# Optimization experiments

Hardware: AMD Instinct MI355X
Metric: run time of the kernel (lower is better)

Reference implementation:

```python
import jax, jax.numpy as jnp
import numpy as np

DIM, HEADS, HEAD_DIM = 1024, 16, 64
B, S = 2, 1024
LAMBDA = 4.0
EPS = 1e-6


def setup_inputs() -> dict:
    key = jax.random.key(0)
    ks = jax.random.split(key, 7)
    sc = 1.0 / np.sqrt(DIM)
    return {
        "x": jax.random.normal(ks[0], (B, S, DIM), jnp.float32),
        "qkv_w": jax.random.normal(ks[1], (3 * DIM, DIM), jnp.float32) * sc,
        "qkv_b": jax.random.normal(ks[2], (3 * DIM,), jnp.float32) * 0.01,
        "proj_w": jax.random.normal(ks[3], (DIM, DIM), jnp.float32) * sc,
        "proj_b": jax.random.normal(ks[4], (DIM,), jnp.float32) * 0.01,
        "dwc_w": jax.random.normal(ks[5], (DIM, 1, 3), jnp.float32) * 0.3,
        "dwc_b": jax.random.normal(ks[6], (DIM,), jnp.float32) * 0.01,
    }


def _l1_dist(q, k):
    # q,k: [B,H,S,Dh] -> pairwise L1 distance [B,H,S,S].
    # Accumulate over head_dim with a (rematerialized) scan so we never
    # materialize the [B,H,S,S,Dh] broadcast tensor.
    qT = jnp.moveaxis(q, -1, 0)  # [Dh,B,H,S]
    kT = jnp.moveaxis(k, -1, 0)

    def step(acc, qk):
        qd, kd = qk  # [B,H,S]
        return acc + jnp.abs(qd[..., :, None] - kd[..., None, :]), None

    init = jnp.zeros(q.shape[:-1] + (k.shape[-2],), q.dtype)
    dist, _ = jax.lax.scan(jax.checkpoint(step), init, (qT, kT))
    return dist


def reference(x, qkv_w, qkv_b, proj_w, proj_b, dwc_w, dwc_b):
    Bq, Sq, C = x.shape
    # qkv projection -> q,k,v each [B,H,S,Dh]
    qkv = (x @ qkv_w.T + qkv_b).reshape(Bq, Sq, 3, HEADS, HEAD_DIM)
    qkv = jnp.transpose(qkv, (2, 0, 3, 1, 4))
    q, k, v = qkv[0], qkv[1], qkv[2]

    # exact Laplacian (L1-distance) kernel attention, row-normalized
    dist = _l1_dist(q, k)                       # [B,H,S,S]
    kern = jnp.exp(-LAMBDA * dist / HEAD_DIM)   # mean-L1 scaling
    attn = kern / (jnp.sum(kern, axis=-1, keepdims=True) + EPS)
    global_attn = jnp.einsum("bhij,bhjd->bhid", attn, v)

    # depthwise conv1d local branch on v (channel order = head-major)
    v1d = jnp.transpose(v, (0, 1, 3, 2)).reshape(Bq, C, Sq)  # [B,C,S]
    local = jax.lax.conv_general_dilated(
        v1d, dwc_w, window_strides=(1,), padding=((1, 1),),
        feature_group_count=C, dimension_numbers=("NCH", "OIH", "NCH"))
    local = local + dwc_b[None, :, None]
    local = jnp.transpose(local.reshape(Bq, HEADS, HEAD_DIM, Sq), (0, 1, 3, 2))

    y = global_attn + local                      # [B,H,S,Dh]
    y = jnp.transpose(y, (0, 2, 1, 3)).reshape(Bq, Sq, C)
    return y @ proj_w.T + proj_b
```

## Files before the change

kernel.cpp:

```cpp
#include <hip/hip_runtime.h>

#define DIMC 1024
#define HEADS 16
#define HD 64
#define BATCH 2
#define SEQ 1024
#define NQKV 3072

typedef _Float16 f16;
typedef _Float16 half8 __attribute__((ext_vector_type(8)));
typedef _Float16 half4v __attribute__((ext_vector_type(4)));
typedef float floatx4 __attribute__((ext_vector_type(4)));

__device__ __forceinline__ void gld16(const void* g, void* l) {
  __builtin_amdgcn_global_load_lds((const __attribute__((address_space(1))) void*)g,
                                   (__attribute__((address_space(3))) void*)l, 16, 0, 0);
}

__device__ __forceinline__ unsigned sadU8(unsigned a, unsigned b, unsigned c) {
#if __has_builtin(__builtin_amdgcn_sad_u8)
  return __builtin_amdgcn_sad_u8(a, b, c);
#else
  unsigned d;
  asm("v_sad_u8 %0, %1, %2, %3" : "=v"(d) : "v"(a), "v"(b), "v"(c));
  return d;
#endif
}

__global__ __launch_bounds__(256) void cvt_kernel(
    const float* __restrict__ x, const float* __restrict__ wq, const float* __restrict__ wp,
    f16* __restrict__ x16, f16* __restrict__ wq16, f16* __restrict__ wp16)
{
  long long bid = blockIdx.x;
  const float* src; f16* dst; long long base;
  if (bid < 2048)            { src = x;  dst = x16;  base = bid; }
  else if (bid < 2048+3072)  { src = wq; dst = wq16; base = bid - 2048; }
  else                       { src = wp; dst = wp16; base = bid - (2048+3072); }
  long long i = base*256 + threadIdx.x;
  float4 v = ((const float4*)src)[i];
  half4v h; h[0]=(f16)v.x; h[1]=(f16)v.y; h[2]=(f16)v.z; h[3]=(f16)v.w;
  *(half4v*)(dst + i*4) = h;
}

template<int MODE>
__global__ __launch_bounds__(256, 2) void gemm_kernel(
    const f16* __restrict__ A, const f16* __restrict__ Bw, const float* __restrict__ bias,
    unsigned char* __restrict__ q8, unsigned char* __restrict__ k8, f16* __restrict__ vT,
    float* __restrict__ outp, int K)
{
  __shared__ f16 As[128*64];
  __shared__ f16 Bs[128*64];
  const int tid = threadIdx.x;
  const int wave = tid >> 6, lane = tid & 63;
  const int lq = lane >> 4, li = lane & 15;
  const int m0 = blockIdx.y * 128, n0 = blockIdx.x * 128;
  const int wm = (wave & 1) * 64, wn = (wave >> 1) * 64;
  floatx4 acc[4][4] = {};

  const int kIters = K / 64;
  for (int kt = 0; kt < kIters; ++kt) {
    __syncthreads();
#pragma unroll
    for (int r = 0; r < 4; ++r) {
      int slot = r*256 + tid;
      int row = slot >> 3, c = slot & 7, sc = c ^ (row & 7);
      gld16(A  + (size_t)(m0+row)*K + kt*64 + sc*8, As + slot*8);
      gld16(Bw + (size_t)(n0+row)*K + kt*64 + sc*8, Bs + slot*8);
    }
    __syncthreads();
#pragma unroll
    for (int ks = 0; ks < 2; ++ks) {
      half8 af[4], bf[4];
#pragma unroll
      for (int t = 0; t < 4; ++t) {
        int am = wm + t*16 + li;
        int kc = ks*4 + lq;
        af[t] = *(const half8*)&As[am*64 + (kc ^ (am & 7))*8];
        int bn = wn + t*16 + li;
        bf[t] = *(const half8*)&Bs[bn*64 + (kc ^ (bn & 7))*8];
      }
#pragma unroll
      for (int mt = 0; mt < 4; ++mt)
#pragma unroll
        for (int nt = 0; nt < 4; ++nt)
          acc[mt][nt] = __builtin_amdgcn_mfma_f32_16x16x32_f16(af[mt], bf[nt], acc[mt][nt], 0, 0, 0);
    }
  }

#pragma unroll
  for (int mt = 0; mt < 4; ++mt) {
#pragma unroll
    for (int nt = 0; nt < 4; ++nt) {
      int f = n0 + wn + nt*16 + li;
      float bb = bias[f];
      if (MODE == 0) {
        int which = f >> 10, cc = f & 1023, h = cc >> 6, d = cc & 63;
        int t0 = m0 + wm + mt*16 + lq*4;
        int b = t0 >> 10, s0 = t0 & 1023;
        if (which == 2) {
          half4v hv;
#pragma unroll
          for (int r = 0; r < 4; ++r) hv[r] = (f16)(acc[mt][nt][r] + bb);
          *(half4v*)&vT[((size_t)((b*HEADS + h)*HD + d))*SEQ + s0] = hv;
        } else {
          unsigned char* dst = (which == 0) ? q8 : k8;
#pragma unroll
          for (int r = 0; r < 4; ++r) {
            float v = acc[mt][nt][r] + bb;
            int u = (int)floorf(v * 16.0f + 128.5f);
            u = u < 0 ? 0 : (u > 255 ? 255 : u);
            dst[((size_t)((b*HEADS + h)*SEQ + s0 + r))*HD + d] = (unsigned char)u;
          }
        }
      } else {
#pragma unroll
        for (int r = 0; r < 4; ++r) {
          int t = m0 + wm + mt*16 + lq*4 + r;
          outp[(size_t)t*DIMC + f] = acc[mt][nt][r] + bb;
        }
      }
    }
  }
}

__global__ __launch_bounds__(256, 2) void attn_kernel(
    const unsigned char* __restrict__ q8g, const unsigned char* __restrict__ k8g,
    const f16* __restrict__ vTg, const float* __restrict__ dwcw, const float* __restrict__ dwcb,
    f16* __restrict__ y16)
{
  __shared__ unsigned char q8s[64*64];
  __shared__ unsigned char k8s[128*64];
  __shared__ f16 vTs[64*128];
  __shared__ f16 sfrag[16*64*8];
  __shared__ float rspart[64*16];
  __shared__ float rowsum[64];
  __shared__ f16 vconv[64*66];

  const int tid = threadIdx.x;
  const int bh = blockIdx.y;
  const int i0 = blockIdx.x * 64;
  const int lane = tid & 63, wave = tid >> 6;
  const int lq = lane >> 4, li = lane & 15;
  const int iL = tid & 15, jt = tid >> 4;
  const int ksj = jt >> 2, qj = jt & 3;

  {
    int row = tid >> 2, c = tid & 3;
    gld16(q8g + ((size_t)(bh*SEQ) + i0 + row)*HD + c*16, q8s + tid*16);
  }
  {
    int d = tid >> 2, part = tid & 3;
    const f16* vrow = vTg + ((size_t)(bh*HD) + d)*SEQ;
#pragma unroll
    for (int e = 0; e < 17; ++e) {
      int ss = part*17 + e;
      if (ss < 66) {
        int s = i0 - 1 + ss;
        vconv[d*66 + ss] = (s >= 0 && s < SEQ) ? vrow[s] : (f16)0.0f;
      }
    }
  }
  __syncthreads();

  unsigned qr[4][16];
#pragma unroll
  for (int n = 0; n < 4; ++n)
#pragma unroll
    for (int c4 = 0; c4 < 4; ++c4) {
      uint4 t = *(const uint4*)&q8s[(iL + n*16)*64 + c4*16];
      qr[n][c4*4+0] = t.x; qr[n][c4*4+1] = t.y; qr[n][c4*4+2] = t.z; qr[n][c4*4+3] = t.w;
    }

  float rs[4] = {0.f, 0.f, 0.f, 0.f};
  floatx4 pacc[2][2] = {};
  const int mtb = (wave & 1) * 2, ntb = (wave >> 1) * 2;

  for (int jb = 0; jb < 8; ++jb) {
    const int j0 = jb * 128;
    __syncthreads();
#pragma unroll
    for (int r = 0; r < 2; ++r) {
      int slot = r*256 + tid;
      int row = slot >> 2, c = slot & 3;
      gld16(k8g + ((size_t)(bh*SEQ) + j0 + row)*HD + c*16, k8s + slot*16);
    }
#pragma unroll
    for (int r = 0; r < 4; ++r) {
      int slot = r*256 + tid;
      int d = slot >> 4, c = slot & 15, sc = c ^ (d & 7);
      gld16(vTg + ((size_t)(bh*HD) + d)*SEQ + j0 + sc*8, vTs + slot*8);
    }
    __syncthreads();

    unsigned sacc[4][8] = {};
#pragma unroll
    for (int c4 = 0; c4 < 4; ++c4) {
      uint4 kk[8];
#pragma unroll
      for (int jj = 0; jj < 8; ++jj)
        kk[jj] = *(const uint4*)&k8s[(jt*8 + jj)*64 + c4*16];
#pragma unroll
      for (int n = 0; n < 4; ++n)
#pragma unroll
        for (int jj = 0; jj < 8; ++jj) {
          sacc[n][jj] = sadU8(qr[n][c4*4+0], kk[jj].x, sacc[n][jj]);
          sacc[n][jj] = sadU8(qr[n][c4*4+1], kk[jj].y, sacc[n][jj]);
          sacc[n][jj] = sadU8(qr[n][c4*4+2], kk[jj].z, sacc[n][jj]);
          sacc[n][jj] = sadU8(qr[n][c4*4+3], kk[jj].w, sacc[n][jj]);
        }
    }
#pragma unroll
    for (int n = 0; n < 4; ++n) {
      half8 sv;
#pragma unroll
      for (int jj = 0; jj < 8; ++jj) {
        float sf = exp2f(-0.0056355275f * (float)sacc[n][jj]);
        rs[n] += sf;
        sv[jj] = (f16)sf;
      }
      *(half8*)&sfrag[((n*4 + ksj)*64 + qj*16 + iL)*8] = sv;
    }
    __syncthreads();

#pragma unroll
    for (int ks = 0; ks < 4; ++ks) {
      half8 a0 = *(const half8*)&sfrag[(((mtb+0)*4 + ks)*64 + lane)*8];
      half8 a1 = *(const half8*)&sfrag[(((mtb+1)*4 + ks)*64 + lane)*8];
#pragma unroll
      for (int nt = 0; nt < 2; ++nt) {
        int d = (ntb + nt)*16 + li;
        int kc = ks*4 + lq;
        half8 bfr = *(const half8*)&vTs[d*128 + (kc ^ (d & 7))*8];
        pacc[0][nt] = __builtin_amdgcn_mfma_f32_16x16x32_f16(a0, bfr, pacc[0][nt], 0, 0, 0);
        pacc[1][nt] = __builtin_amdgcn_mfma_f32_16x16x32_f16(a1, bfr, pacc[1][nt], 0, 0, 0);
      }
    }
  }

#pragma unroll
  for (int n = 0; n < 4; ++n) rspart[(iL + n*16)*16 + jt] = rs[n];
  __syncthreads();
  if (tid < 64) {
    float s = 0.f;
#pragma unroll
    for (int t = 0; t < 16; ++t) s += rspart[tid*16 + t];
    rowsum[tid] = s + 1e-6f;
  }
  __syncthreads();

  const int b = bh >> 4, h = bh & 15;
#pragma unroll
  for (int nt = 0; nt < 2; ++nt) {
    int d = (ntb + nt)*16 + li;
    int c = h*64 + d;
    float w0 = dwcw[c*3+0], w1 = dwcw[c*3+1], w2 = dwcw[c*3+2], cb = dwcb[c];
#pragma unroll
    for (int mt = 0; mt < 2; ++mt)
#pragma unroll
      for (int r = 0; r < 4; ++r) {
        int ii = (mtb + mt)*16 + lq*4 + r;
        float val = pacc[mt][nt][r] / rowsum[ii];
        val += w0*(float)vconv[d*66 + ii] + w1*(float)vconv[d*66 + ii + 1]
             + w2*(float)vconv[d*66 + ii + 2] + cb;
        int s = i0 + ii;
        y16[((size_t)(b*SEQ + s))*DIMC + c] = (f16)val;
      }
  }
}

extern "C" void kernel_launch(void* const* d_in, const int* in_sizes, int n_in,
                              void* d_out, int out_size, void* d_ws, size_t ws_size,
                              hipStream_t stream) {
  const float* x      = (const float*)d_in[0];
  const float* qkv_w  = (const float*)d_in[1];
  const float* qkv_b  = (const float*)d_in[2];
  const float* proj_w = (const float*)d_in[3];
  const float* proj_b = (const float*)d_in[4];
  const float* dwc_w  = (const float*)d_in[5];
  const float* dwc_b  = (const float*)d_in[6];
  float* out = (float*)d_out;

  char* ws = (char*)d_ws;
  f16* x16  = (f16*)(ws);
  f16* wq16 = (f16*)(ws + (4ll<<20));
  f16* wp16 = (f16*)(ws + (10ll<<20));
  unsigned char* q8 = (unsigned char*)(ws + (12ll<<20));
  unsigned char* k8 = (unsigned char*)(ws + (14ll<<20));
  f16* vT   = (f16*)(ws + (16ll<<20));
  f16* y16  = (f16*)(ws + (20ll<<20));

  cvt_kernel<<<6144, 256, 0, stream>>>(x, qkv_w, proj_w, x16, wq16, wp16);
  gemm_kernel<0><<<dim3(24, 16), 256, 0, stream>>>(x16, wq16, qkv_b, q8, k8, vT, nullptr, DIMC);
  attn_kernel<<<dim3(16, 32), 256, 0, stream>>>(q8, k8, vT, dwc_w, dwc_b, y16);
  gemm_kernel<1><<<dim3(8, 16), 256, 0, stream>>>(y16, wp16, proj_b, nullptr, nullptr, nullptr, out, DIMC);
}
```

Before: 163.3 us.

## Split attention keys across waves with double-buffered staging; shrink GEMM tiles

The attention kernel now gives each wave its own quarter of the key sequence. K/V tiles are double-buffered with per-wave async loads and explicit waitcnt instead of block-wide barriers. Score fragments go straight from registers into MFMA operands rather than through shared memory, and per-wave partial outputs and row sums are combined with LDS atomics at the end. The GEMMs are templated on tile size and use smaller 64x128 and 64x64 tiles with higher occupancy bounds, to fill more CUs. The cost is an LDS atomic reduction over 64x64 floats, reloading q from LDS on every step, and more register pressure from the 4x4 accumulators.

After: 194.1 us. 18.9% more time.

```diff
diff --git a/kernel.cpp b/kernel.cpp
--- a/kernel.cpp
+++ b/kernel.cpp
@@ -42,55 +42,65 @@
   *(half4v*)(dst + i*4) = h;
 }
 
-template<int MODE>
-__global__ __launch_bounds__(256, 2) void gemm_kernel(
+template<int TM, int TN, int MODE>
+__global__ __launch_bounds__(256, 4) void gemm_kernel(
     const f16* __restrict__ A, const f16* __restrict__ Bw, const float* __restrict__ bias,
     unsigned char* __restrict__ q8, unsigned char* __restrict__ k8, f16* __restrict__ vT,
     float* __restrict__ outp, int K)
 {
-  __shared__ f16 As[128*64];
-  __shared__ f16 Bs[128*64];
+  constexpr int MT = TM / 32;
+  constexpr int NT = TN / 32;
+  __shared__ f16 As[TM*64];
+  __shared__ f16 Bs[TN*64];
   const int tid = threadIdx.x;
   const int wave = tid >> 6, lane = tid & 63;
   const int lq = lane >> 4, li = lane & 15;
-  const int m0 = blockIdx.y * 128, n0 = blockIdx.x * 128;
-  const int wm = (wave & 1) * 64, wn = (wave >> 1) * 64;
-  floatx4 acc[4][4] = {};
+  const int m0 = blockIdx.y * TM, n0 = blockIdx.x * TN;
+  const int wm = (wave & 1) * (TM/2), wn = (wave >> 1) * (TN/2);
+  floatx4 acc[MT][NT] = {};
 
   const int kIters = K / 64;
   for (int kt = 0; kt < kIters; ++kt) {
     __syncthreads();
 #pragma unroll
-    for (int r = 0; r < 4; ++r) {
+    for (int r = 0; r < TM/32; ++r) {
       int slot = r*256 + tid;
       int row = slot >> 3, c = slot & 7, sc = c ^ (row & 7);
-      gld16(A  + (size_t)(m0+row)*K + kt*64 + sc*8, As + slot*8);
+      gld16(A + (size_t)(m0+row)*K + kt*64 + sc*8, As + slot*8);
+    }
+#pragma unroll
+    for (int r = 0; r < TN/32; ++r) {
+      int slot = r*256 + tid;
+      int row = slot >> 3, c = slot & 7, sc = c ^ (row & 7);
       gld16(Bw + (size_t)(n0+row)*K + kt*64 + sc*8, Bs + slot*8);
     }
     __syncthreads();
 #pragma unroll
     for (int ks = 0; ks < 2; ++ks) {
-      half8 af[4], bf[4];
-#pragma unroll
-      for (int t = 0; t < 4; ++t) {
+      half8 af[MT], bf[NT];
+      int kc = ks*4 + lq;
+#pragma unroll
+      for (int t = 0; t < MT; ++t) {
         int am = wm + t*16 + li;
-        int kc = ks*4 + lq;
         af[t] = *(const half8*)&As[am*64 + (kc ^ (am & 7))*8];
+      }
+#pragma unroll
+      for (int t = 0; t < NT; ++t) {
         int bn = wn + t*16 + li;
         bf[t] = *(const half8*)&Bs[bn*64 + (kc ^ (bn & 7))*8];
       }
 #pragma unroll
-      for (int mt = 0; mt < 4; ++mt)
-#pragma unroll
-        for (int nt = 0; nt < 4; ++nt)
+      for (int mt = 0; mt < MT; ++mt)
+#pragma unroll
+        for (int nt = 0; nt < NT; ++nt)
           acc[mt][nt] = __builtin_amdgcn_mfma_f32_16x16x32_f16(af[mt], bf[nt], acc[mt][nt], 0, 0, 0);
     }
   }
 
 #pragma unroll
-  for (int mt = 0; mt < 4; ++mt) {
-#pragma unroll
-    for (int nt = 0; nt < 4; ++nt) {
+  for (int mt = 0; mt < MT; ++mt) {
+#pragma unroll
+    for (int nt = 0; nt < NT; ++nt) {
       int f = n0 + wn + nt*16 + li;
       float bb = bias[f];
       if (MODE == 0) {
@@ -129,11 +139,10 @@
     f16* __restrict__ y16)
 {
   __shared__ unsigned char q8s[64*64];
-  __shared__ unsigned char k8s[128*64];
-  __shared__ f16 vTs[64*128];
-  __shared__ f16 sfrag[16*64*8];
-  __shared__ float rspart[64*16];
-  __shared__ float rowsum[64];
+  __shared__ unsigned char k8s[2][4][32*64];
+  __shared__ f16 vTs[2][4][64*32];
+  __shared__ float Obuf[64*64];
+  __shared__ float rowsumS[64];
   __shared__ f16 vconv[64*66];
 
   const int tid = threadIdx.x;
@@ -141,13 +150,13 @@
   const int i0 = blockIdx.x * 64;
   const int lane = tid & 63, wave = tid >> 6;
   const int lq = lane >> 4, li = lane & 15;
-  const int iL = tid & 15, jt = tid >> 4;
-  const int ksj = jt >> 2, qj = jt & 3;
-
-  {
-    int row = tid >> 2, c = tid & 3;
-    gld16(q8g + ((size_t)(bh*SEQ) + i0 + row)*HD + c*16, q8s + tid*16);
-  }
+
+#pragma unroll
+  for (int i = 0; i < 16; ++i) Obuf[tid + i*256] = 0.0f;
+  if (tid < 64) rowsumS[tid] = 1e-6f;
+
+  gld16(q8g + ((size_t)bh*SEQ + i0)*HD + tid*16, q8s + tid*16);
+
   {
     int d = tid >> 2, part = tid & 3;
     const f16* vrow = vTg + ((size_t)(bh*HD) + d)*SEQ;
@@ -160,112 +169,122 @@
       }
     }
   }
+
+  auto stage = [&](int buf, int jb) {
+    int j0w = wave*256 + jb*32;
+    const unsigned char* kg = k8g + ((size_t)bh*SEQ + j0w)*HD;
+    unsigned char* kd = &k8s[buf][wave][0];
+    gld16(kg + lane*16,        kd + lane*16);
+    gld16(kg + 1024 + lane*16, kd + 1024 + lane*16);
+    f16* vd = &vTs[buf][wave][0];
+#pragma unroll
+    for (int i4 = 0; i4 < 4; ++i4) {
+      int d = i4*16 + (lane >> 2), c = lane & 3;
+      int g = c ^ ((d >> 1) & 3);
+      gld16(vTg + ((size_t)(bh*HD) + d)*SEQ + j0w + g*8, vd + i4*512 + lane*8);
+    }
+  };
+
+  stage(0, 0);
   __syncthreads();
 
-  unsigned qr[4][16];
-#pragma unroll
-  for (int n = 0; n < 4; ++n)
-#pragma unroll
-    for (int c4 = 0; c4 < 4; ++c4) {
-      uint4 t = *(const uint4*)&q8s[(iL + n*16)*64 + c4*16];
-      qr[n][c4*4+0] = t.x; qr[n][c4*4+1] = t.y; qr[n][c4*4+2] = t.z; qr[n][c4*4+3] = t.w;
-    }
-
   float rs[4] = {0.f, 0.f, 0.f, 0.f};
-  floatx4 pacc[2][2] = {};
-  const int mtb = (wave & 1) * 2, ntb = (wave >> 1) * 2;
+  floatx4 pacc[4][4] = {};
 
   for (int jb = 0; jb < 8; ++jb) {
-    const int j0 = jb * 128;
-    __syncthreads();
-#pragma unroll
-    for (int r = 0; r < 2; ++r) {
-      int slot = r*256 + tid;
-      int row = slot >> 2, c = slot & 3;
-      gld16(k8g + ((size_t)(bh*SEQ) + j0 + row)*HD + c*16, k8s + slot*16);
-    }
-#pragma unroll
-    for (int r = 0; r < 4; ++r) {
-      int slot = r*256 + tid;
-      int d = slot >> 4, c = slot & 15, sc = c ^ (d & 7);
-      gld16(vTg + ((size_t)(bh*HD) + d)*SEQ + j0 + sc*8, vTs + slot*8);
-    }
-    __syncthreads();
+    int cur = jb & 1;
+    if (jb < 7) {
+      stage(cur ^ 1, jb + 1);
+      __builtin_amdgcn_sched_barrier(0);
+      __builtin_amdgcn_s_waitcnt(0x0F76);
+    } else {
+      __builtin_amdgcn_sched_barrier(0);
+      __builtin_amdgcn_s_waitcnt(0x0F70);
+    }
+    __builtin_amdgcn_sched_barrier(0);
+
+    const unsigned char* kb = &k8s[cur][wave][0];
+    const f16* vb = &vTs[cur][wave][0];
 
     unsigned sacc[4][8] = {};
 #pragma unroll
-    for (int c4 = 0; c4 < 4; ++c4) {
+    for (int p = 0; p < 4; ++p) {
+      int cc = (p + lq) & 3;
       uint4 kk[8];
 #pragma unroll
       for (int jj = 0; jj < 8; ++jj)
-        kk[jj] = *(const uint4*)&k8s[(jt*8 + jj)*64 + c4*16];
+        kk[jj] = *(const uint4*)&kb[(lq*8 + jj)*64 + cc*16];
+      uint4 qc[4];
 #pragma unroll
       for (int n = 0; n < 4; ++n)
+        qc[n] = *(const uint4*)&q8s[(li + n*16)*64 + cc*16];
+#pragma unroll
+      for (int n = 0; n < 4; ++n)
 #pragma unroll
         for (int jj = 0; jj < 8; ++jj) {
-          sacc[n][jj] = sadU8(qr[n][c4*4+0], kk[jj].x, sacc[n][jj]);
-          sacc[n][jj] = sadU8(qr[n][c4*4+1], kk[jj].y, sacc[n][jj]);
-          sacc[n][jj] = sadU8(qr[n][c4*4+2], kk[jj].z, sacc[n][jj]);
-          sacc[n][jj] = sadU8(qr[n][c4*4+3], kk[jj].w, sacc[n][jj]);
+          sacc[n][jj] = sadU8(qc[n].x, kk[jj].x, sacc[n][jj]);
+          sacc[n][jj] = sadU8(qc[n].y, kk[jj].y, sacc[n][jj]);
+          sacc[n][jj] = sadU8(qc[n].z, kk[jj].z, sacc[n][jj]);
+          sacc[n][jj] = sadU8(qc[n].w, kk[jj].w, sacc[n][jj]);
         }
     }
-#pragma unroll
-    for (int n = 0; n < 4; ++n) {
-      half8 sv;
+
+    half8 af[4];
+#pragma unroll
+    for (int n = 0; n < 4; ++n)
 #pragma unroll
       for (int jj = 0; jj < 8; ++jj) {
         float sf = exp2f(-0.0056355275f * (float)sacc[n][jj]);
         rs[n] += sf;
-        sv[jj] = (f16)sf;
-      }
-      *(half8*)&sfrag[((n*4 + ksj)*64 + qj*16 + iL)*8] = sv;
-    }
-    __syncthreads();
-
-#pragma unroll
-    for (int ks = 0; ks < 4; ++ks) {
-      half8 a0 = *(const half8*)&sfrag[(((mtb+0)*4 + ks)*64 + lane)*8];
-      half8 a1 = *(const half8*)&sfrag[(((mtb+1)*4 + ks)*64 + lane)*8];
-#pragma unroll
-      for (int nt = 0; nt < 2; ++nt) {
-        int d = (ntb + nt)*16 + li;
-        int kc = ks*4 + lq;
-        half8 bfr = *(const half8*)&vTs[d*128 + (kc ^ (d & 7))*8];
-        pacc[0][nt] = __builtin_amdgcn_mfma_f32_16x16x32_f16(a0, bfr, pacc[0][nt], 0, 0, 0);
-        pacc[1][nt] = __builtin_amdgcn_mfma_f32_16x16x32_f16(a1, bfr, pacc[1][nt], 0, 0, 0);
-      }
-    }
-  }
-
-#pragma unroll
-  for (int n = 0; n < 4; ++n) rspart[(iL + n*16)*16 + jt] = rs[n];
+        af[n][jj] = (f16)sf;
+      }
+
+#pragma unroll
+    for (int nt = 0; nt < 4; ++nt) {
+      int d = nt*16 + li;
+      half8 bfr = *(const half8*)&vb[d*32 + ((lq ^ ((d >> 1) & 3)) * 8)];
+#pragma unroll
+      for (int mt = 0; mt < 4; ++mt)
+        pacc[mt][nt] = __builtin_amdgcn_mfma_f32_16x16x32_f16(af[mt], bfr, pacc[mt][nt], 0, 0, 0);
+    }
+  }
+
+#pragma unroll
+  for (int n = 0; n < 4; ++n) {
+    rs[n] += __shfl_xor(rs[n], 16, 64);
+    rs[n] += __shfl_xor(rs[n], 32, 64);
+  }
+  if (lane < 16) {
+#pragma unroll
+    for (int n = 0; n < 4; ++n) atomicAdd(&rowsumS[lane + n*16], rs[n]);
+  }
+#pragma unroll
+  for (int mt = 0; mt < 4; ++mt)
+#pragma unroll
+    for (int nt = 0; nt < 4; ++nt)
+#pragma unroll
+      for (int r = 0; r < 4; ++r)
+        atomicAdd(&Obuf[(mt*16 + lq*4 + r)*64 + nt*16 + li], pacc[mt][nt][r]);
   __syncthreads();
-  if (tid < 64) {
-    float s = 0.f;
-#pragma unroll
-    for (int t = 0; t < 16; ++t) s += rspart[tid*16 + t];
-    rowsum[tid] = s + 1e-6f;
-  }
-  __syncthreads();
 
   const int b = bh >> 4, h = bh & 15;
-#pragma unroll
-  for (int nt = 0; nt < 2; ++nt) {
-    int d = (ntb + nt)*16 + li;
+  const int r = tid >> 2, dq = tid & 3;
+  float inv = 1.0f / rowsumS[r];
+  half8 hv0, hv1;
+#pragma unroll
+  for (int e = 0; e < 16; ++e) {
+    int d = dq*16 + e;
     int c = h*64 + d;
-    float w0 = dwcw[c*3+0], w1 = dwcw[c*3+1], w2 = dwcw[c*3+2], cb = dwcb[c];
-#pragma unroll
-    for (int mt = 0; mt < 2; ++mt)
-#pragma unroll
-      for (int r = 0; r < 4; ++r) {
-        int ii = (mtb + mt)*16 + lq*4 + r;
-        float val = pacc[mt][nt][r] / rowsum[ii];
-        val += w0*(float)vconv[d*66 + ii] + w1*(float)vconv[d*66 + ii + 1]
-             + w2*(float)vconv[d*66 + ii + 2] + cb;
-        int s = i0 + ii;
-        y16[((size_t)(b*SEQ + s))*DIMC + c] = (f16)val;
-      }
-  }
+    float val = Obuf[r*64 + d] * inv
+              + dwcw[c*3+0] * (float)vconv[d*66 + r]
+              + dwcw[c*3+1] * (float)vconv[d*66 + r + 1]
+              + dwcw[c*3+2] * (float)vconv[d*66 + r + 2]
+              + dwcb[c];
+    if (e < 8) hv0[e] = (f16)val; else hv1[e-8] = (f16)val;
+  }
+  f16* yp = y16 + ((size_t)(b*SEQ + i0 + r))*DIMC + h*64 + dq*16;
+  *(half8*)yp = hv0;
+  *(half8*)(yp + 8) = hv1;
 }
 
 extern "C" void kernel_launch(void* const* d_in, const int* in_sizes, int n_in,
@@ -290,7 +309,7 @@
   f16* y16  = (f16*)(ws + (20ll<<20));
 
   cvt_kernel<<<6144, 256, 0, stream>>>(x, qkv_w, proj_w, x16, wq16, wp16);
-  gemm_kernel<0><<<dim3(24, 16), 256, 0, stream>>>(x16, wq16, qkv_b, q8, k8, vT, nullptr, DIMC);
+  gemm_kernel<64,128,0><<<dim3(24, 32), 256, 0, stream>>>(x16, wq16, qkv_b, q8, k8, vT, nullptr, DIMC);
   attn_kernel<<<dim3(16, 32), 256, 0, stream>>>(q8, k8, vT, dwc_w, dwc_b, y16);
-  gemm_kernel<1><<<dim3(8, 16), 256, 0, stream>>>(y16, wp16, proj_b, nullptr, nullptr, nullptr, out, DIMC);
-}
+  gemm_kernel<64,64,1><<<dim3(16, 32), 256, 0, stream>>>(y16, wp16, proj_b, nullptr, nullptr, nullptr, out, DIMC);
+}
```

## Shrink GEMM and attention tiles for more blocks; read V fragments directly from global

Applied to the files above, without the earlier changes.

Templates the GEMM on tile sizes and launches smaller tiles (64x128 for QKV, 64x64 for the projection) with a higher occupancy hint. This raises block count on a many-CU GPU. The attention kernel halves the query rows per block to 32, doubling the grid. It drops the LDS staging of V, so MFMA B-fragments are loaded straight from global memory. The aim is better CU utilisation and less LDS use, at the cost of more redundant K/V reads and uncoalesced global loads inside the MFMA loop.

Result: no change. 162.0 us (-0.8%).

```diff
diff --git a/kernel.cpp b/kernel.cpp
--- a/kernel.cpp
+++ b/kernel.cpp
@@ -42,55 +42,65 @@
   *(half4v*)(dst + i*4) = h;
 }
 
-template<int MODE>
-__global__ __launch_bounds__(256, 2) void gemm_kernel(
+template<int TM, int TN, int MODE>
+__global__ __launch_bounds__(256, 4) void gemm_kernel(
     const f16* __restrict__ A, const f16* __restrict__ Bw, const float* __restrict__ bias,
     unsigned char* __restrict__ q8, unsigned char* __restrict__ k8, f16* __restrict__ vT,
     float* __restrict__ outp, int K)
 {
-  __shared__ f16 As[128*64];
-  __shared__ f16 Bs[128*64];
+  constexpr int MT = TM / 32;
+  constexpr int NT = TN / 32;
+  __shared__ f16 As[TM*64];
+  __shared__ f16 Bs[TN*64];
   const int tid = threadIdx.x;
   const int wave = tid >> 6, lane = tid & 63;
   const int lq = lane >> 4, li = lane & 15;
-  const int m0 = blockIdx.y * 128, n0 = blockIdx.x * 128;
-  const int wm = (wave & 1) * 64, wn = (wave >> 1) * 64;
-  floatx4 acc[4][4] = {};
+  const int m0 = blockIdx.y * TM, n0 = blockIdx.x * TN;
+  const int wm = (wave & 1) * (TM/2), wn = (wave >> 1) * (TN/2);
+  floatx4 acc[MT][NT] = {};
 
   const int kIters = K / 64;
   for (int kt = 0; kt < kIters; ++kt) {
     __syncthreads();
 #pragma unroll
-    for (int r = 0; r < 4; ++r) {
+    for (int r = 0; r < TM/32; ++r) {
       int slot = r*256 + tid;
       int row = slot >> 3, c = slot & 7, sc = c ^ (row & 7);
-      gld16(A  + (size_t)(m0+row)*K + kt*64 + sc*8, As + slot*8);
+      gld16(A + (size_t)(m0+row)*K + kt*64 + sc*8, As + slot*8);
+    }
+#pragma unroll
+    for (int r = 0; r < TN/32; ++r) {
+      int slot = r*256 + tid;
+      int row = slot >> 3, c = slot & 7, sc = c ^ (row & 7);
       gld16(Bw + (size_t)(n0+row)*K + kt*64 + sc*8, Bs + slot*8);
     }
     __syncthreads();
 #pragma unroll
     for (int ks = 0; ks < 2; ++ks) {
-      half8 af[4], bf[4];
-#pragma unroll
-      for (int t = 0; t < 4; ++t) {
+      half8 af[MT], bf[NT];
+      int kc = ks*4 + lq;
+#pragma unroll
+      for (int t = 0; t < MT; ++t) {
         int am = wm + t*16 + li;
-        int kc = ks*4 + lq;
         af[t] = *(const half8*)&As[am*64 + (kc ^ (am & 7))*8];
+      }
+#pragma unroll
+      for (int t = 0; t < NT; ++t) {
         int bn = wn + t*16 + li;
         bf[t] = *(const half8*)&Bs[bn*64 + (kc ^ (bn & 7))*8];
       }
 #pragma unroll
-      for (int mt = 0; mt < 4; ++mt)
-#pragma unroll
-        for (int nt = 0; nt < 4; ++nt)
+      for (int mt = 0; mt < MT; ++mt)
+#pragma unroll
+        for (int nt = 0; nt < NT; ++nt)
           acc[mt][nt] = __builtin_amdgcn_mfma_f32_16x16x32_f16(af[mt], bf[nt], acc[mt][nt], 0, 0, 0);
     }
   }
 
 #pragma unroll
-  for (int mt = 0; mt < 4; ++mt) {
-#pragma unroll
-    for (int nt = 0; nt < 4; ++nt) {
+  for (int mt = 0; mt < MT; ++mt) {
+#pragma unroll
+    for (int nt = 0; nt < NT; ++nt) {
       int f = n0 + wn + nt*16 + li;
       float bb = bias[f];
       if (MODE == 0) {
@@ -123,57 +133,55 @@
   }
 }
 
-__global__ __launch_bounds__(256, 2) void attn_kernel(
+__global__ __launch_bounds__(256, 4) void attn_kernel(
     const unsigned char* __restrict__ q8g, const unsigned char* __restrict__ k8g,
     const f16* __restrict__ vTg, const float* __restrict__ dwcw, const float* __restrict__ dwcb,
     f16* __restrict__ y16)
 {
-  __shared__ unsigned char q8s[64*64];
+  __shared__ unsigned char q8s[32*64];
   __shared__ unsigned char k8s[128*64];
-  __shared__ f16 vTs[64*128];
-  __shared__ f16 sfrag[16*64*8];
-  __shared__ float rspart[64*16];
-  __shared__ float rowsum[64];
-  __shared__ f16 vconv[64*66];
+  __shared__ f16 sfrag[8*64*8];
+  __shared__ float rspart[32*16];
+  __shared__ float rowsumS[32];
+  __shared__ f16 vconv[64*34];
 
   const int tid = threadIdx.x;
   const int bh = blockIdx.y;
-  const int i0 = blockIdx.x * 64;
+  const int i0 = blockIdx.x * 32;
   const int lane = tid & 63, wave = tid >> 6;
   const int lq = lane >> 4, li = lane & 15;
   const int iL = tid & 15, jt = tid >> 4;
   const int ksj = jt >> 2, qj = jt & 3;
-
-  {
-    int row = tid >> 2, c = tid & 3;
-    gld16(q8g + ((size_t)(bh*SEQ) + i0 + row)*HD + c*16, q8s + tid*16);
-  }
+  const int mtb = wave & 1, ntb = wave >> 1;
+
+  if (wave < 2)
+    gld16(q8g + ((size_t)bh*SEQ + i0)*HD + tid*16, q8s + tid*16);
+
   {
     int d = tid >> 2, part = tid & 3;
     const f16* vrow = vTg + ((size_t)(bh*HD) + d)*SEQ;
 #pragma unroll
-    for (int e = 0; e < 17; ++e) {
-      int ss = part*17 + e;
-      if (ss < 66) {
+    for (int e = 0; e < 9; ++e) {
+      int ss = part*9 + e;
+      if (ss < 34) {
         int s = i0 - 1 + ss;
-        vconv[d*66 + ss] = (s >= 0 && s < SEQ) ? vrow[s] : (f16)0.0f;
+        vconv[d*34 + ss] = (s >= 0 && s < SEQ) ? vrow[s] : (f16)0.0f;
       }
     }
   }
   __syncthreads();
 
-  unsigned qr[4][16];
-#pragma unroll
-  for (int n = 0; n < 4; ++n)
+  unsigned qr[2][16];
+#pragma unroll
+  for (int n = 0; n < 2; ++n)
 #pragma unroll
     for (int c4 = 0; c4 < 4; ++c4) {
       uint4 t = *(const uint4*)&q8s[(iL + n*16)*64 + c4*16];
       qr[n][c4*4+0] = t.x; qr[n][c4*4+1] = t.y; qr[n][c4*4+2] = t.z; qr[n][c4*4+3] = t.w;
     }
 
-  float rs[4] = {0.f, 0.f, 0.f, 0.f};
-  floatx4 pacc[2][2] = {};
-  const int mtb = (wave & 1) * 2, ntb = (wave >> 1) * 2;
+  float rs[2] = {0.f, 0.f};
+  floatx4 pacc[2] = {};
 
   for (int jb = 0; jb < 8; ++jb) {
     const int j0 = jb * 128;
@@ -181,18 +189,11 @@
 #pragma unroll
     for (int r = 0; r < 2; ++r) {
       int slot = r*256 + tid;
-      int row = slot >> 2, c = slot & 3;
-      gld16(k8g + ((size_t)(bh*SEQ) + j0 + row)*HD + c*16, k8s + slot*16);
-    }
-#pragma unroll
-    for (int r = 0; r < 4; ++r) {
-      int slot = r*256 + tid;
-      int d = slot >> 4, c = slot & 15, sc = c ^ (d & 7);
-      gld16(vTg + ((size_t)(bh*HD) + d)*SEQ + j0 + sc*8, vTs + slot*8);
-    }
-    __syncthreads();
-
-    unsigned sacc[4][8] = {};
+      gld16(k8g + ((size_t)bh*SEQ + j0)*HD + slot*16, k8s + slot*16);
+    }
+    __syncthreads();
+
+    unsigned sacc[2][8] = {};
 #pragma unroll
     for (int c4 = 0; c4 < 4; ++c4) {
       uint4 kk[8];
@@ -200,7 +201,7 @@
       for (int jj = 0; jj < 8; ++jj)
         kk[jj] = *(const uint4*)&k8s[(jt*8 + jj)*64 + c4*16];
 #pragma unroll
-      for (int n = 0; n < 4; ++n)
+      for (int n = 0; n < 2; ++n)
 #pragma unroll
         for (int jj = 0; jj < 8; ++jj) {
           sacc[n][jj] = sadU8(qr[n][c4*4+0], kk[jj].x, sacc[n][jj]);
@@ -210,7 +211,7 @@
         }
     }
 #pragma unroll
-    for (int n = 0; n < 4; ++n) {
+    for (int n = 0; n < 2; ++n) {
       half8 sv;
 #pragma unroll
       for (int jj = 0; jj < 8; ++jj) {
@@ -224,47 +225,42 @@
 
 #pragma unroll
     for (int ks = 0; ks < 4; ++ks) {
-      half8 a0 = *(const half8*)&sfrag[(((mtb+0)*4 + ks)*64 + lane)*8];
-      half8 a1 = *(const half8*)&sfrag[(((mtb+1)*4 + ks)*64 + lane)*8];
+      half8 a = *(const half8*)&sfrag[((mtb*4 + ks)*64 + lane)*8];
 #pragma unroll
       for (int nt = 0; nt < 2; ++nt) {
-        int d = (ntb + nt)*16 + li;
-        int kc = ks*4 + lq;
-        half8 bfr = *(const half8*)&vTs[d*128 + (kc ^ (d & 7))*8];
-        pacc[0][nt] = __builtin_amdgcn_mfma_f32_16x16x32_f16(a0, bfr, pacc[0][nt], 0, 0, 0);
-        pacc[1][nt] = __builtin_amdgcn_mfma_f32_16x16x32_f16(a1, bfr, pacc[1][nt], 0, 0, 0);
-      }
-    }
-  }
-
-#pragma unroll
-  for (int n = 0; n < 4; ++n) rspart[(iL + n*16)*16 + jt] = rs[n];
+        int d = (ntb*2 + nt)*16 + li;
+        half8 bfr = *(const half8*)(vTg + ((size_t)(bh*HD) + d)*SEQ + j0 + (ks*4 + lq)*8);
+        pacc[nt] = __builtin_amdgcn_mfma_f32_16x16x32_f16(a, bfr, pacc[nt], 0, 0, 0);
+      }
+    }
+  }
+
+#pragma unroll
+  for (int n = 0; n < 2; ++n) rspart[(iL + n*16)*16 + jt] = rs[n];
   __syncthreads();
-  if (tid < 64) {
+  if (tid < 32) {
     float s = 0.f;
 #pragma unroll
     for (int t = 0; t < 16; ++t) s += rspart[tid*16 + t];
-    rowsum[tid] = s + 1e-6f;
+    rowsumS[tid] = s + 1e-6f;
   }
   __syncthreads();
 
   const int b = bh >> 4, h = bh & 15;
 #pragma unroll
   for (int nt = 0; nt < 2; ++nt) {
-    int d = (ntb + nt)*16 + li;
+    int d = (ntb*2 + nt)*16 + li;
     int c = h*64 + d;
     float w0 = dwcw[c*3+0], w1 = dwcw[c*3+1], w2 = dwcw[c*3+2], cb = dwcb[c];
 #pragma unroll
-    for (int mt = 0; mt < 2; ++mt)
-#pragma unroll
-      for (int r = 0; r < 4; ++r) {
-        int ii = (mtb + mt)*16 + lq*4 + r;
-        float val = pacc[mt][nt][r] / rowsum[ii];
-        val += w0*(float)vconv[d*66 + ii] + w1*(float)vconv[d*66 + ii + 1]
-             + w2*(float)vconv[d*66 + ii + 2] + cb;
-        int s = i0 + ii;
-        y16[((size_t)(b*SEQ + s))*DIMC + c] = (f16)val;
-      }
+    for (int r = 0; r < 4; ++r) {
+      int ii = mtb*16 + lq*4 + r;
+      float val = pacc[nt][r] / rowsumS[ii];
+      val += w0*(float)vconv[d*34 + ii] + w1*(float)vconv[d*34 + ii + 1]
+           + w2*(float)vconv[d*34 + ii + 2] + cb;
+      int s = i0 + ii;
+      y16[((size_t)(b*SEQ + s))*DIMC + c] = (f16)val;
+    }
   }
 }
 
@@ -290,7 +286,7 @@
   f16* y16  = (f16*)(ws + (20ll<<20));
 
   cvt_kernel<<<6144, 256, 0, stream>>>(x, qkv_w, proj_w, x16, wq16, wp16);
-  gemm_kernel<0><<<dim3(24, 16), 256, 0, stream>>>(x16, wq16, qkv_b, q8, k8, vT, nullptr, DIMC);
-  attn_kernel<<<dim3(16, 32), 256, 0, stream>>>(q8, k8, vT, dwc_w, dwc_b, y16);
-  gemm_kernel<1><<<dim3(8, 16), 256, 0, stream>>>(y16, wp16, proj_b, nullptr, nullptr, nullptr, out, DIMC);
-}
+  gemm_kernel<64,128,0><<<dim3(24, 32), 256, 0, stream>>>(x16, wq16, qkv_b, q8, k8, vT, nullptr, DIMC);
+  attn_kernel<<<dim3(32, 32), 256, 0, stream>>>(q8, k8, vT, dwc_w, dwc_b, y16);
+  gemm_kernel<64,64,1><<<dim3(16, 32), 256, 0, stream>>>(y16, wp16, proj_b, nullptr, nullptr, nullptr, out, DIMC);
+}
```
